# Optimization experiments

Hardware: AMD Instinct MI355X
Metric: run time of the kernel (lower is better)

The kernel has to match this reference:

```python
import jax, jax.numpy as jnp
import numpy as np

D_MODEL = 1024
N_HEADS = 16
HEAD_DIM = D_MODEL // N_HEADS
FFN = 4096
NUM_REL = 64
BATCH = 4
SEQ = 1024
EPS = 1e-6


def _layernorm(x, g, b):
    mu = jnp.mean(x, axis=-1, keepdims=True)
    var = jnp.mean(jnp.square(x - mu), axis=-1, keepdims=True)
    return (x - mu) * jax.lax.rsqrt(var + EPS) * g + b


def setup_inputs() -> dict:
    key = jax.random.key(0)
    ks = jax.random.split(key, 16)
    s_d = 1.0 / np.sqrt(D_MODEL)
    s_f = 1.0 / np.sqrt(FFN)
    inp = {
        "x": jax.random.normal(ks[0], (BATCH, SEQ, D_MODEL), jnp.float32),
        "relative_ids": jax.random.randint(ks[1], (SEQ, SEQ), 0, NUM_REL),
        # attention projections (row-major: y = x @ W + b)
        "Wq": jax.random.normal(ks[2], (D_MODEL, D_MODEL), jnp.float32) * s_d,
        "bq": jnp.zeros((D_MODEL,), jnp.float32),
        "Wk": jax.random.normal(ks[3], (D_MODEL, D_MODEL), jnp.float32) * s_d,
        "bk": jnp.zeros((D_MODEL,), jnp.float32),
        "Wv": jax.random.normal(ks[4], (D_MODEL, D_MODEL), jnp.float32) * s_d,
        "bv": jnp.zeros((D_MODEL,), jnp.float32),
        "Wo": jax.random.normal(ks[5], (D_MODEL, D_MODEL), jnp.float32) * s_d,
        "bo": jnp.zeros((D_MODEL,), jnp.float32),
        # relative position tables: Ek for keys (rel-e), Eb per-head bias (rel-b)
        "Ek": jax.random.normal(ks[6], (NUM_REL, HEAD_DIM), jnp.float32) * (1.0 / np.sqrt(HEAD_DIM)),
        "Eb": jax.random.normal(ks[7], (NUM_REL, N_HEADS), jnp.float32) * 0.02,
        # layernorms
        "g1": jnp.ones((D_MODEL,), jnp.float32),
        "b1": jnp.zeros((D_MODEL,), jnp.float32),
        "g2": jnp.ones((D_MODEL,), jnp.float32),
        "b2": jnp.zeros((D_MODEL,), jnp.float32),
        # FFN
        "W1": jax.random.normal(ks[8], (D_MODEL, FFN), jnp.float32) * s_d,
        "bf1": jnp.zeros((FFN,), jnp.float32),
        "W2": jax.random.normal(ks[9], (FFN, D_MODEL), jnp.float32) * s_f,
        "bf2": jnp.zeros((D_MODEL,), jnp.float32),
    }
    return inp


def _forward(x, relative_ids, Wq, bq, Wk, bk, Wv, bv, Wo, bo, Ek, Eb,
             g1, b1, g2, b2, W1, bf1, W2, bf2):
    B, S, D = x.shape
    # projections -> [B, H, S, Dh]
    def split_heads(t):
        return t.reshape(B, S, N_HEADS, HEAD_DIM).transpose(0, 2, 1, 3)
    q = split_heads(x @ Wq + bq)
    k = split_heads(x @ Wk + bk)
    v = split_heads(x @ Wv + bv)

    scores = jnp.einsum('bhqd,bhkd->bhqk', q, k)
    # rel-e: relative key embeddings interact with queries
    Erel = Ek[relative_ids]                      # [S, S, Dh]
    scores = scores + jnp.einsum('bhqd,qkd->bhqk', q, Erel)
    # rel-b: per-head relative bias
    scores = scores + Eb[relative_ids].transpose(2, 0, 1)[None]  # [1,H,S,S]
    scores = scores / jnp.sqrt(jnp.asarray(HEAD_DIM, x.dtype))

    attn = jax.nn.softmax(scores, axis=-1)
    ctx = jnp.einsum('bhqk,bhkd->bhqd', attn, v)
    ctx = ctx.transpose(0, 2, 1, 3).reshape(B, S, D)
    a_out = ctx @ Wo + bo

    # dropout is identity at eval
    ff_in = _layernorm(x + a_out, g1, b1)
    ff = jax.nn.relu(ff_in @ W1 + bf1) @ W2 + bf2
    return _layernorm(ff_in + ff, g2, b2)


def reference(x, relative_ids, Wq, bq, Wk, bk, Wv, bv, Wo, bo, Ek, Eb,
              g1, b1, g2, b2, W1, bf1, W2, bf2):
    return _forward(x, relative_ids, Wq, bq, Wk, bk, Wv, bv, Wo, bo, Ek, Eb,
                    g1, b1, g2, b2, W1, bf1, W2, bf2)
```

## Files before the change

### kernel.cpp

```cpp
#include <hip/hip_runtime.h>


typedef short bf16x8 __attribute__((ext_vector_type(8)));
typedef float f32x4 __attribute__((ext_vector_type(4)));

#define DEVI static __device__ __forceinline__

constexpr int SEQ = 1024, DMODEL = 1024, NH = 16, HDIM = 64, FFDIM = 4096, NREL = 64, NBATCH = 4;
constexpr int ROWS = NBATCH * SEQ;
#define QSC 0.18033688011112042f

DEVI unsigned short f2b(float f) {
  union { float f; unsigned u; } v; v.f = f;
  unsigned r = v.u + 0x7FFFu + ((v.u >> 16) & 1u);
  return (unsigned short)(r >> 16);
}

DEVI float b2f(unsigned short u) {
  union { unsigned v; float f; } x; x.v = (unsigned)u << 16; return x.f;
}

#if __has_builtin(__builtin_amdgcn_cvt_pk_bf16_f32)
DEVI unsigned pack2(float a, float b) {
  auto r = __builtin_amdgcn_cvt_pk_bf16_f32(a, b);
  return __builtin_bit_cast(unsigned, r);
}
#else
DEVI unsigned pack2(float a, float b) {
  return (unsigned)f2b(a) | ((unsigned)f2b(b) << 16);
}
#endif

DEVI float fexp2(float x) {
#if __has_builtin(__builtin_amdgcn_exp2f)
  return __builtin_amdgcn_exp2f(x);
#else
  return exp2f(x);
#endif
}

DEVI float4 ld4h(const unsigned short* p) {
  uint2 u = *(const uint2*)p;
  union { unsigned v; float f; } a, b, c, d;
  a.v = u.x << 16; b.v = u.x & 0xffff0000u; c.v = u.y << 16; d.v = u.y & 0xffff0000u;
  return make_float4(a.f, b.f, c.f, d.f);
}

DEVI void gload16(const unsigned short* g, unsigned short* l) {
  __builtin_amdgcn_global_load_lds((const __attribute__((address_space(1))) void*)g,
                                   (__attribute__((address_space(3))) void*)l, 16, 0, 0);
}

template <int BM, int BN, int WR, int WC>
DEVI void gemm_core(const unsigned short* __restrict__ A, int lda,
                    const unsigned short* __restrict__ Bt, int ldb, int K,
                    unsigned short* sA, unsigned short* sB, f32x4* acc) {
  constexpr int BK = 64;
  constexpr int MT = BM / (WR * 16), NT = BN / (WC * 16);
  const int tid = threadIdx.x;
  const int wave = tid >> 6, lane = tid & 63;
  const int wm = wave % WR, wn = wave / WR;
  const int lr = lane & 15, kq = lane >> 4;
  const int srow = lane >> 3;
  const int schunk = (lane & 7) ^ (srow & 7);
  const int sw = lr & 7;

  const f32x4 zero = {0.f, 0.f, 0.f, 0.f};
#pragma unroll
  for (int i = 0; i < MT * NT; ++i) acc[i] = zero;

  const unsigned short* ga = A + (size_t)(wave * (BM / 4) + srow) * lda + schunk * 8;
  const unsigned short* gb = Bt + (size_t)(wave * (BN / 4) + srow) * ldb + schunk * 8;
  unsigned short* la = sA + wave * (BM / 4) * BK;
  unsigned short* lb = sB + wave * (BN / 4) * BK;
  const unsigned short* pa = sA + (wm * MT * 16 + lr) * BK;
  const unsigned short* pb = sB + (wn * NT * 16 + lr) * BK;

  for (int k0 = 0; k0 < K; k0 += BK) {
#pragma unroll
    for (int j = 0; j < BM / 32; ++j) gload16(ga + (size_t)(j * 8) * lda + k0, la + j * 8 * BK);
#pragma unroll
    for (int j = 0; j < BN / 32; ++j) gload16(gb + (size_t)(j * 8) * ldb + k0, lb + j * 8 * BK);
    __syncthreads();
#pragma unroll
    for (int ks = 0; ks < 2; ++ks) {
      const int rc = ((ks * 4 + kq) ^ sw) * 8;
      bf16x8 af[MT], bv[NT];
#pragma unroll
      for (int mi = 0; mi < MT; ++mi) af[mi] = *(const bf16x8*)(pa + mi * 16 * BK + rc);
#pragma unroll
      for (int ni = 0; ni < NT; ++ni) bv[ni] = *(const bf16x8*)(pb + ni * 16 * BK + rc);
#pragma unroll
      for (int mi = 0; mi < MT; ++mi)
#pragma unroll
        for (int ni = 0; ni < NT; ++ni)
          acc[mi * NT + ni] =
              __builtin_amdgcn_mfma_f32_16x16x32_bf16(af[mi], bv[ni], acc[mi * NT + ni], 0, 0, 0);
    }
    __syncthreads();
  }
}

#define EPI_VARS                                     \
  const int tid = threadIdx.x;                       \
  const int wave = tid >> 6, lane = tid & 63;        \
  const int wm = wave % WR, wn = wave / WR;          \
  const int lr = lane & 15, kq = lane >> 4;

__global__ __launch_bounds__(256) void k_proj_qkv(
    const unsigned short* __restrict__ A, const unsigned short* __restrict__ WqT,
    const unsigned short* __restrict__ WkT, const unsigned short* __restrict__ WvT,
    const float* __restrict__ bq, const float* __restrict__ bk, const float* __restrict__ bv,
    unsigned short* __restrict__ oq, unsigned short* __restrict__ ok,
    unsigned short* __restrict__ ov) {
  constexpr int BM = 128, BN = 128, WR = 2, WC = 2, MT = 4, NT = 4;
  __shared__ __align__(16) unsigned short sA[BM * 64];
  __shared__ __align__(16) unsigned short sB[BN * 64];
  f32x4 acc[MT * NT];
  const int which = blockIdx.z;
  const unsigned short* Bt = which == 0 ? WqT : which == 1 ? WkT : WvT;
  const float* bias = which == 0 ? bq : which == 1 ? bk : bv;
  unsigned short* out = which == 0 ? oq : which == 1 ? ok : ov;
  const float scl = which == 0 ? QSC : 1.0f;
  const int m0 = blockIdx.y * BM, n0 = blockIdx.x * BN;
  gemm_core<BM, BN, WR, WC>(A + (size_t)m0 * DMODEL, DMODEL, Bt + (size_t)n0 * DMODEL, DMODEL,
                            DMODEL, sA, sB, acc);
  EPI_VARS
#pragma unroll
  for (int mi = 0; mi < MT; ++mi) {
    const int row0 = m0 + wm * MT * 16 + mi * 16 + kq * 4;
    const int b = row0 >> 10, s0 = row0 & 1023;
#pragma unroll
    for (int ni = 0; ni < NT; ++ni) {
      const int col = n0 + wn * NT * 16 + ni * 16 + lr;
      const int h = col >> 6, d = col & 63;
      const float bc = bias[col];
      f32x4 v = acc[mi * NT + ni];
#pragma unroll
      for (int r = 0; r < 4; ++r) v[r] = (v[r] + bc) * scl;
      if (which != 2) {
#pragma unroll
        for (int r = 0; r < 4; ++r)
          out[((size_t)((b * NH + h) * SEQ) + s0 + r) * HDIM + d] = f2b(v[r]);
      } else {
        uint2 p = make_uint2(pack2(v[0], v[1]), pack2(v[2], v[3]));
        *(uint2*)&out[((size_t)((b * NH + h) * HDIM) + d) * SEQ + s0] = p;
      }
    }
  }
}

template <int BM, int BN, int WR, int WC, bool RELU, bool OUTBF16, bool SPLITK = false>
__global__ __launch_bounds__(256) void k_gemm(const unsigned short* __restrict__ A, int lda,
                                              const unsigned short* __restrict__ Bt, int ldb, int K,
                                              int N, const float* __restrict__ bias,
                                              float* __restrict__ outf,
                                              unsigned short* __restrict__ outh,
                                              size_t ostride = 0) {
  constexpr int MT = BM / (WR * 16), NT = BN / (WC * 16);
  __shared__ __align__(16) unsigned short sA[BM * 64];
  __shared__ __align__(16) unsigned short sB[BN * 64];
  f32x4 acc[MT * NT];
  const int m0 = blockIdx.y * BM, n0 = blockIdx.x * BN;
  const int kc = SPLITK ? blockIdx.z : 0;
  gemm_core<BM, BN, WR, WC>(A + (size_t)m0 * lda + (size_t)kc * K, lda,
                            Bt + (size_t)n0 * ldb + (size_t)kc * K, ldb, K, sA, sB, acc);
  if (SPLITK) outh += (size_t)kc * ostride;
  EPI_VARS
#pragma unroll
  for (int mi = 0; mi < MT; ++mi) {
    const int row0 = m0 + wm * MT * 16 + mi * 16 + kq * 4;
#pragma unroll
    for (int ni = 0; ni < NT; ++ni) {
      const int col = n0 + wn * NT * 16 + ni * 16 + lr;
      const float bc = (bias && (!SPLITK || kc == 0)) ? bias[col] : 0.f;
      f32x4 v = acc[mi * NT + ni];
#pragma unroll
      for (int r = 0; r < 4; ++r) {
        float y = v[r] + bc;
        if (RELU) y = fmaxf(y, 0.f);
        if (OUTBF16 || SPLITK)
          outh[(size_t)(row0 + r) * N + col] = f2b(y);
        else
          outf[(size_t)(row0 + r) * N + col] = y;
      }
    }
  }
}

__global__ __launch_bounds__(256, 4) void k_flash(const unsigned short* __restrict__ q,
                                                  const unsigned short* __restrict__ kk,
                                                  const unsigned short* __restrict__ vT,
                                                  const unsigned short* __restrict__ Ekb,
                                                  const float* __restrict__ Eb,
                                                  const unsigned char* __restrict__ rel8,
                                                  unsigned short* __restrict__ ctx) {
  __shared__ __align__(16) unsigned short sK[128 * 64];
  __shared__ __align__(16) unsigned short sV[64 * 128];
  __shared__ __align__(16) unsigned short sqEB16[64 * 62];
  __shared__ float sRow[4][16];

  const int tid = threadIdx.x, wave = tid >> 6, lane = tid & 63;
  const int lr = lane & 15, kq = lane >> 4;

  const int L = blockIdx.y * 16 + blockIdx.x;
  const int xcd = L & 7, idx = L >> 3;
  const int z = xcd * 8 + (idx >> 4), qt = idx & 15;
  const int b = z >> 4, h = z & 15;
  const size_t zo = (size_t)z * SEQ * HDIM;
  const size_t vo = (size_t)z * HDIM * SEQ;

  const int srow8 = lane >> 3, sl8 = lane & 7;
  const int sw8 = sl8 ^ (srow8 & 7);
  const int dl = lane >> 4, sl16 = lane & 15;
  const int swl = lr & 7;
  const f32x4 zero = {0.f, 0.f, 0.f, 0.f};

  unsigned short* sQv = sV;
#pragma unroll
  for (int j = 0; j < 2; ++j) {
    const int row = wave * 16 + j * 8 + srow8;
    gload16(q + zo + (size_t)(qt * 64 + row) * 64 + sw8 * 8, sQv + (wave * 16 + j * 8) * 64);
    gload16(Ekb + (size_t)row * 64 + sw8 * 8, sK + (wave * 16 + j * 8) * 64);
  }
  __syncthreads();

  bf16x8 bq_[2];
#pragma unroll
  for (int ks = 0; ks < 2; ++ks)
    bq_[ks] = *(const bf16x8*)&sQv[(wave * 16 + lr) * 64 + (((ks * 4 + kq) ^ swl) << 3)];

  {
    f32x4 accE[4];
#pragma unroll
    for (int nf = 0; nf < 4; ++nf) accE[nf] = zero;
#pragma unroll
    for (int ks = 0; ks < 2; ++ks) {
#pragma unroll
      for (int nf = 0; nf < 4; ++nf) {
        bf16x8 ek = *(const bf16x8*)&sK[(nf * 16 + lr) * 64 + (((ks * 4 + kq) ^ swl) << 3)];
        accE[nf] = __builtin_amdgcn_mfma_f32_16x16x32_bf16(bq_[ks], ek, accE[nf], 0, 0, 0);
      }
    }
#pragma unroll
    for (int nf = 0; nf < 4; ++nf) {
      const int rid = nf * 16 + lr;
      const float eb = Eb[rid * NH + h] * QSC;
      const int base = rid * 62 + wave * 16 + kq * 4;
      *(unsigned*)&sqEB16[base] = pack2(accE[nf][0] + eb, accE[nf][1] + eb);
      *(unsigned*)&sqEB16[base + 2] = pack2(accE[nf][2] + eb, accE[nf][3] + eb);
    }
  }

  float l_run = 0.f;
  f32x4 accO[4];
#pragma unroll
  for (int nd = 0; nd < 4; ++nd) accO[nd] = zero;
  const int qrow_g = qt * 64 + wave * 16 + lr;
  const unsigned char* relrow8 = rel8 + (size_t)qrow_g * SEQ;
  const int qcol = wave * 16 + lr;
  unsigned short* sPw = sK + wave * 2048;

  for (int kt = 0; kt < 8; ++kt) {
    __syncthreads();
#pragma unroll
    for (int j = 0; j < 4; ++j) {
      const int row = wave * 32 + j * 8 + srow8;
      gload16(kk + zo + (size_t)(kt * 128 + row) * 64 + sw8 * 8, sK + (wave * 32 + j * 8) * 64);
    }
#pragma unroll
    for (int j = 0; j < 4; ++j) {
      const int row = wave * 16 + j * 4 + dl;
      const int ch = sl16 ^ (row & 15);
      gload16(vT + vo + (size_t)row * SEQ + kt * 128 + ch * 8, sV + (wave * 16 + j * 4) * 128);
    }
    unsigned ru[8];
#pragma unroll
    for (int mi = 0; mi < 8; ++mi)
      ru[mi] = *(const unsigned*)&relrow8[kt * 128 + mi * 16 + kq * 4];
    __syncthreads();

    f32x4 accS[8];
#pragma unroll
    for (int mi = 0; mi < 8; ++mi) accS[mi] = zero;
#pragma unroll
    for (int ks = 0; ks < 2; ++ks) {
#pragma unroll
      for (int mi = 0; mi < 8; ++mi) {
        bf16x8 a = *(const bf16x8*)&sK[(mi * 16 + lr) * 64 + (((ks * 4 + kq) ^ swl) << 3)];
        accS[mi] = __builtin_amdgcn_mfma_f32_16x16x32_bf16(a, bq_[ks], accS[mi], 0, 0, 0);
      }
    }
#pragma unroll
    for (int mi = 0; mi < 8; ++mi) {
      const float p0 = fexp2(accS[mi][0] + b2f(sqEB16[(int)(ru[mi] & 255u) * 62 + qcol]));
      const float p1 = fexp2(accS[mi][1] + b2f(sqEB16[(int)((ru[mi] >> 8) & 255u) * 62 + qcol]));
      const float p2 = fexp2(accS[mi][2] + b2f(sqEB16[(int)((ru[mi] >> 16) & 255u) * 62 + qcol]));
      const float p3 = fexp2(accS[mi][3] + b2f(sqEB16[(int)(ru[mi] >> 24) * 62 + qcol]));
      accS[mi][0] = p0; accS[mi][1] = p1; accS[mi][2] = p2; accS[mi][3] = p3;
      l_run += (p0 + p1) + (p2 + p3);
    }
    __syncthreads();

#pragma unroll
    for (int mi = 0; mi < 8; ++mi) {
      const int c = 2 * mi + (kq >> 1);
      *(uint2*)&sPw[lr * 128 + ((c ^ lr) << 3) + ((kq & 1) << 2)] =
          make_uint2(pack2(accS[mi][0], accS[mi][1]), pack2(accS[mi][2], accS[mi][3]));
    }
#pragma unroll
    for (int kst = 0; kst < 4; ++kst) {
      const int cc = ((kq + 4 * kst) ^ lr) << 3;
      bf16x8 a = *(const bf16x8*)&sPw[lr * 128 + cc];
#pragma unroll
      for (int nd = 0; nd < 4; ++nd) {
        bf16x8 bv = *(const bf16x8*)&sV[(nd * 16 + lr) * 128 + cc];
        accO[nd] = __builtin_amdgcn_mfma_f32_16x16x32_bf16(a, bv, accO[nd], 0, 0, 0);
      }
    }
  }

  l_run += __shfl_xor(l_run, 16);
  l_run += __shfl_xor(l_run, 32);
  if (kq == 0) sRow[wave][lr] = l_run;
  const float4 lv = *(const float4*)&sRow[wave][kq * 4];
  const float inv[4] = {1.f / lv.x, 1.f / lv.y, 1.f / lv.z, 1.f / lv.w};
  const size_t rbase = (size_t)(b * SEQ + qt * 64 + wave * 16 + kq * 4);
#pragma unroll
  for (int nd = 0; nd < 4; ++nd) {
    const int col = h * HDIM + nd * 16 + lr;
#pragma unroll
    for (int r = 0; r < 4; ++r)
      ctx[(rbase + r) * DMODEL + col] = f2b(accO[nd][r] * inv[r]);
  }
}

template <bool WB>
__global__ __launch_bounds__(256) void k_addln3(const unsigned short* __restrict__ a,
                                                const unsigned short* __restrict__ p0,
                                                const unsigned short* __restrict__ p1,
                                                const float* __restrict__ g,
                                                const float* __restrict__ beta,
                                                float* __restrict__ outf,
                                                unsigned short* __restrict__ outh) {
  const int row = blockIdx.x, t = threadIdx.x;
  const size_t base = (size_t)row * DMODEL + t * 4;
  float4 va = ld4h(&a[base]);
  float4 v0 = ld4h(&p0[base]);
  float4 v1 = ld4h(&p1[base]);
  const float x0 = va.x + v0.x + v1.x, x1 = va.y + v0.y + v1.y;
  const float x2 = va.z + v0.z + v1.z, x3 = va.w + v0.w + v1.w;
  __shared__ float red[4];
  float s = x0 + x1 + x2 + x3;
#pragma unroll
  for (int o = 32; o; o >>= 1) s += __shfl_xor(s, o);
  if ((t & 63) == 0) red[t >> 6] = s;
  __syncthreads();
  const float mu = (red[0] + red[1] + red[2] + red[3]) * (1.0f / DMODEL);
  __syncthreads();
  const float d0 = x0 - mu, d1 = x1 - mu, d2 = x2 - mu, d3 = x3 - mu;
  float qv = d0 * d0 + d1 * d1 + d2 * d2 + d3 * d3;
#pragma unroll
  for (int o = 32; o; o >>= 1) qv += __shfl_xor(qv, o);
  if ((t & 63) == 0) red[t >> 6] = qv;
  __syncthreads();
  const float var = (red[0] + red[1] + red[2] + red[3]) * (1.0f / DMODEL);
  const float sc = rsqrtf(var + 1e-6f);
  float4 vg = *(const float4*)&g[t * 4];
  float4 ve = *(const float4*)&beta[t * 4];
  float4 y;
  y.x = d0 * sc * vg.x + ve.x;
  y.y = d1 * sc * vg.y + ve.y;
  y.z = d2 * sc * vg.z + ve.z;
  y.w = d3 * sc * vg.w + ve.w;
  if (WB) {
    uint2 p = make_uint2(pack2(y.x, y.y), pack2(y.z, y.w));
    *(uint2*)&outh[base] = p;
  } else {
    *(float4*)&outf[base] = y;
  }
}

__global__ __launch_bounds__(256) void k_tcast12(
    const float* __restrict__ Wq, const float* __restrict__ Wk, const float* __restrict__ Wv,
    const float* __restrict__ Wo, const float* __restrict__ W1, const float* __restrict__ W2,
    unsigned short* __restrict__ oq, unsigned short* __restrict__ ok,
    unsigned short* __restrict__ ov, unsigned short* __restrict__ oo,
    unsigned short* __restrict__ o1, unsigned short* __restrict__ o2) {
  const int z = blockIdx.z;
  const float* in;
  unsigned short* out;
  int ldi, ldo;
  if (z < 4) {
    in = z == 0 ? Wq : z == 1 ? Wk : z == 2 ? Wv : Wo;
    out = z == 0 ? oq : z == 1 ? ok : z == 2 ? ov : oo;
    ldi = 1024; ldo = 1024;
  } else if (z < 8) {
    const int s = z - 4;
    in = W1 + (size_t)s * 1024; ldi = 4096;
    out = o1 + (size_t)s * 1024 * 1024; ldo = 1024;
  } else {
    const int s = z - 8;
    in = W2 + (size_t)s * 1024 * 1024; ldi = 1024;
    out = o2 + (size_t)s * 1024; ldo = 4096;
  }
  __shared__ float tile[32][33];
  const int tx = threadIdx.x & 31, ty = threadIdx.x >> 5;
  const int r0 = blockIdx.y * 32, c0 = blockIdx.x * 32;
#pragma unroll
  for (int i = 0; i < 4; ++i)
    tile[ty + i * 8][tx] = in[(size_t)(r0 + ty + i * 8) * ldi + c0 + tx];
  __syncthreads();
#pragma unroll
  for (int i = 0; i < 4; ++i)
    out[(size_t)(c0 + ty + i * 8) * ldo + r0 + tx] = f2b(tile[tx][ty + i * 8]);
}

__global__ __launch_bounds__(256) void k_cast2(const float* __restrict__ a,
                                               unsigned short* __restrict__ oa, int n4a,
                                               const float* __restrict__ bsrc,
                                               unsigned short* __restrict__ ob, int n4b,
                                               const int* __restrict__ rel,
                                               unsigned char* __restrict__ r8, int n4c) {
  const int i = blockIdx.x * 256 + threadIdx.x;
  if (i < n4a) {
    float4 v = *(const float4*)&a[(size_t)i * 4];
    uint2 p = make_uint2(pack2(v.x, v.y), pack2(v.z, v.w));
    *(uint2*)&oa[(size_t)i * 4] = p;
  } else {
    const int j = i - n4a;
    if (j < n4b) {
      float4 v = *(const float4*)&bsrc[(size_t)j * 4];
      uint2 p = make_uint2(pack2(v.x, v.y), pack2(v.z, v.w));
      *(uint2*)&ob[(size_t)j * 4] = p;
    } else {
      const int k2 = j - n4b;
      if (k2 < n4c) {
        int4 v = *(const int4*)&rel[(size_t)k2 * 4];
        unsigned pk = (unsigned)(v.x & 255) | ((unsigned)(v.y & 255) << 8) |
                      ((unsigned)(v.z & 255) << 16) | ((unsigned)(v.w & 255) << 24);
        *(unsigned*)&r8[(size_t)k2 * 4] = pk;
      }
    }
  }
}


extern "C" void kernel_launch(void* const* d_in, const int* in_sizes, int n_in, void* d_out,
                              int out_size, void* d_ws, size_t ws_size, hipStream_t stream) {
  const float* x = (const float*)d_in[0];
  const int* rel = (const int*)d_in[1];
  const float* Wq = (const float*)d_in[2];
  const float* bq = (const float*)d_in[3];
  const float* Wk = (const float*)d_in[4];
  const float* bk = (const float*)d_in[5];
  const float* Wv = (const float*)d_in[6];
  const float* bv = (const float*)d_in[7];
  const float* Wo = (const float*)d_in[8];
  const float* bo = (const float*)d_in[9];
  const float* Ek = (const float*)d_in[10];
  const float* Eb = (const float*)d_in[11];
  const float* g1 = (const float*)d_in[12];
  const float* b1 = (const float*)d_in[13];
  const float* g2 = (const float*)d_in[14];
  const float* b2 = (const float*)d_in[15];
  const float* W1 = (const float*)d_in[16];
  const float* bf1 = (const float*)d_in[17];
  const float* W2 = (const float*)d_in[18];
  const float* bf2 = (const float*)d_in[19];
  float* out = (float*)d_out;

  char* ws = (char*)d_ws;
  const size_t MB = 1ull << 20;
  unsigned short* Wqt = (unsigned short*)(ws + 0 * MB);
  unsigned short* Wkt = (unsigned short*)(ws + 2 * MB);
  unsigned short* Wvt = (unsigned short*)(ws + 4 * MB);
  unsigned short* Wot = (unsigned short*)(ws + 6 * MB);
  unsigned short* W1t = (unsigned short*)(ws + 8 * MB);
  unsigned short* W2t = (unsigned short*)(ws + 16 * MB);
  unsigned short* xb = (unsigned short*)(ws + 24 * MB);
  unsigned short* Ekb = (unsigned short*)(ws + 32 * MB);
  unsigned short* qbuf = (unsigned short*)(ws + 33 * MB);
  unsigned short* kbuf = (unsigned short*)(ws + 41 * MB);
  unsigned short* vTb = (unsigned short*)(ws + 49 * MB);
  unsigned short* ctx = (unsigned short*)(ws + 57 * MB);
  unsigned short* Pb = (unsigned short*)(ws + 65 * MB);
  unsigned char* rel8 = (unsigned char*)(ws + 65 * MB);
  unsigned short* ff_in_b = (unsigned short*)(ws + 81 * MB);
  unsigned short* hidden = (unsigned short*)(ws + 89 * MB);
  const size_t OST = (size_t)ROWS * DMODEL;

  k_tcast12<<<dim3(32, 32, 12), 256, 0, stream>>>(Wq, Wk, Wv, Wo, W1, W2, Wqt, Wkt, Wvt, Wot,
                                                  W1t, W2t);
  k_cast2<<<5124, 256, 0, stream>>>(x, xb, ROWS * DMODEL / 4, Ek, Ekb, NREL * HDIM / 4, rel, rel8,
                                    SEQ * SEQ / 4);

  k_proj_qkv<<<dim3(8, 32, 3), 256, 0, stream>>>(xb, Wqt, Wkt, Wvt, bq, bk, bv, qbuf, kbuf, vTb);

  k_flash<<<dim3(16, 64), 256, 0, stream>>>(qbuf, kbuf, vTb, Ekb, Eb, rel8, ctx);

  k_gemm<128, 128, 2, 2, false, true, true><<<dim3(8, 32, 2), 256, 0, stream>>>(
      ctx, DMODEL, Wot, DMODEL, DMODEL / 2, DMODEL, bo, nullptr, Pb, OST);
  k_addln3<true><<<ROWS, 256, 0, stream>>>(xb, Pb, Pb + OST, g1, b1, nullptr, ff_in_b);

  k_gemm<128, 128, 2, 2, true, true><<<dim3(32, 32), 256, 0, stream>>>(
      ff_in_b, DMODEL, W1t, DMODEL, DMODEL, FFDIM, bf1, nullptr, hidden);
  k_gemm<128, 128, 2, 2, false, true, true><<<dim3(8, 32, 2), 256, 0, stream>>>(
      hidden, FFDIM, W2t, FFDIM, FFDIM / 2, DMODEL, bf2, nullptr, Pb, OST);
  k_addln3<false><<<ROWS, 256, 0, stream>>>(ff_in_b, Pb, Pb + OST, g2, b2, out, nullptr);
}
```

Before: 374.2 us.

## Use 256x256-tile, 8-wave GEMM kernel for FFN up-projection

Result: faster. 354.2 us (-5.3%).

```diff
diff --git a/kernel.cpp b/kernel.cpp
--- a/kernel.cpp
+++ b/kernel.cpp
@@ -184,6 +184,94 @@
         else
           outf[(size_t)(row0 + r) * N + col] = y;
       }
+    }
+  }
+}
+
+__global__ __launch_bounds__(512, 2) void k_gemm256(const unsigned short* __restrict__ A, int lda,
+                                                    const unsigned short* __restrict__ Bt, int ldb,
+                                                    int K, int N, const float* __restrict__ bias,
+                                                    unsigned short* __restrict__ outh) {
+  constexpr int MT = 8, NT = 4;
+  __shared__ __align__(16) unsigned short S[2 * 32768];
+  f32x4 acc[MT * NT];
+  const int tid = threadIdx.x, wave = tid >> 6, lane = tid & 63;
+  const int wm = wave & 1, wn = wave >> 1;
+  const int lr = lane & 15, kq = lane >> 4;
+  const int srow = lane >> 3, schunk = (lane & 7) ^ (srow & 7);
+  const int sw = lr & 7;
+  const int m0 = blockIdx.y * 256, n0 = blockIdx.x * 256;
+
+  const f32x4 zero = {0.f, 0.f, 0.f, 0.f};
+#pragma unroll
+  for (int i = 0; i < MT * NT; ++i) acc[i] = zero;
+
+  const unsigned short* ga = A + (size_t)(m0 + wave * 32 + srow) * lda + schunk * 8;
+  const unsigned short* gb = Bt + (size_t)(n0 + wave * 32 + srow) * ldb + schunk * 8;
+  unsigned short* dA = S + (wave * 32) * 64;
+  unsigned short* dB = S + 16384 + (wave * 32) * 64;
+
+#define STAGE256(buf, k0)                                                              \
+  do {                                                                                 \
+    unsigned short* _a = dA + (buf) * 32768;                                           \
+    unsigned short* _b = dB + (buf) * 32768;                                           \
+    _Pragma("unroll") for (int j = 0; j < 4; ++j)                                      \
+        gload16(ga + (size_t)(j * 8) * lda + (k0), _a + j * 8 * 64);                   \
+    _Pragma("unroll") for (int j = 0; j < 4; ++j)                                      \
+        gload16(gb + (size_t)(j * 8) * ldb + (k0), _b + j * 8 * 64);                   \
+  } while (0)
+
+  STAGE256(0, 0);
+  STAGE256(1, 64);
+
+  const unsigned short* pa = S + (wm * 128 + lr) * 64;
+  const unsigned short* pb = S + 16384 + (wn * 64 + lr) * 64;
+  const int nt = K >> 6;
+
+  for (int t = 0; t < nt; ++t) {
+    const int buf = t & 1;
+    if (t < nt - 1) {
+      asm volatile("s_waitcnt vmcnt(8)" ::: "memory");
+    } else {
+      asm volatile("s_waitcnt vmcnt(0)" ::: "memory");
+    }
+    __builtin_amdgcn_s_barrier();
+    asm volatile("" ::: "memory");
+    const unsigned short* qa = pa + buf * 32768;
+    const unsigned short* qb = pb + buf * 32768;
+#pragma unroll
+    for (int ks = 0; ks < 2; ++ks) {
+      const int rc = ((ks * 4 + kq) ^ sw) * 8;
+      bf16x8 af[MT], bv[NT];
+#pragma unroll
+      for (int mi = 0; mi < MT; ++mi) af[mi] = *(const bf16x8*)(qa + mi * 16 * 64 + rc);
+#pragma unroll
+      for (int ni = 0; ni < NT; ++ni) bv[ni] = *(const bf16x8*)(qb + ni * 16 * 64 + rc);
+#pragma unroll
+      for (int mi = 0; mi < MT; ++mi)
+#pragma unroll
+        for (int ni = 0; ni < NT; ++ni)
+          acc[mi * NT + ni] =
+              __builtin_amdgcn_mfma_f32_16x16x32_bf16(af[mi], bv[ni], acc[mi * NT + ni], 0, 0, 0);
+    }
+    asm volatile("" ::: "memory");
+    __builtin_amdgcn_s_barrier();
+    asm volatile("" ::: "memory");
+    if (t + 2 < nt) STAGE256(buf, (t + 2) * 64);
+  }
+#undef STAGE256
+
+#pragma unroll
+  for (int mi = 0; mi < MT; ++mi) {
+    const int row0 = m0 + wm * 128 + mi * 16 + kq * 4;
+#pragma unroll
+    for (int ni = 0; ni < NT; ++ni) {
+      const int col = n0 + wn * 64 + ni * 16 + lr;
+      const float bc = bias[col];
+      f32x4 v = acc[mi * NT + ni];
+#pragma unroll
+      for (int r = 0; r < 4; ++r)
+        outh[(size_t)(row0 + r) * N + col] = f2b(fmaxf(v[r] + bc, 0.f));
     }
   }
 }
@@ -503,8 +591,8 @@
       ctx, DMODEL, Wot, DMODEL, DMODEL / 2, DMODEL, bo, nullptr, Pb, OST);
   k_addln3<true><<<ROWS, 256, 0, stream>>>(xb, Pb, Pb + OST, g1, b1, nullptr, ff_in_b);
 
-  k_gemm<128, 128, 2, 2, true, true><<<dim3(32, 32), 256, 0, stream>>>(
-      ff_in_b, DMODEL, W1t, DMODEL, DMODEL, FFDIM, bf1, nullptr, hidden);
+  k_gemm256<<<dim3(FFDIM / 256, ROWS / 256), 512, 0, stream>>>(ff_in_b, DMODEL, W1t, DMODEL,
+                                                               DMODEL, FFDIM, bf1, hidden);
   k_gemm<128, 128, 2, 2, false, true, true><<<dim3(8, 32, 2), 256, 0, stream>>>(
       hidden, FFDIM, W2t, FFDIM, FFDIM / 2, DMODEL, bf2, nullptr, Pb, OST);
   k_addln3<false><<<ROWS, 256, 0, stream>>>(ff_in_b, Pb, Pb + OST, g2, b2, out, nullptr);
```

## Replace GEMM core with double-buffered 256-row, 8-wave tiles using async LDS loads

Applied to the files above, without the earlier changes.

New measurement: 342.1 us. 1.09x faster.

```diff
diff --git a/kernel.cpp b/kernel.cpp
--- a/kernel.cpp
+++ b/kernel.cpp
@@ -51,45 +51,66 @@
                                    (__attribute__((address_space(3))) void*)l, 16, 0, 0);
 }
 
-template <int BM, int BN, int WR, int WC>
-DEVI void gemm_core(const unsigned short* __restrict__ A, int lda,
+template <int BM, int BN>
+DEVI void g256_core(const unsigned short* __restrict__ A, int lda,
                     const unsigned short* __restrict__ Bt, int ldb, int K,
-                    unsigned short* sA, unsigned short* sB, f32x4* acc) {
-  constexpr int BK = 64;
-  constexpr int MT = BM / (WR * 16), NT = BN / (WC * 16);
-  const int tid = threadIdx.x;
-  const int wave = tid >> 6, lane = tid & 63;
-  const int wm = wave % WR, wn = wave / WR;
+                    unsigned short* S, f32x4* acc) {
+  constexpr int MT = BM / 32, NT = BN / 64;
+  constexpr int LOADS = BM / 64 + BN / 64;
+  constexpr int SBUF = (BM + BN) * 64;
+  const int tid = threadIdx.x, wave = tid >> 6, lane = tid & 63;
+  const int wm = wave & 1, wn = wave >> 1;
   const int lr = lane & 15, kq = lane >> 4;
-  const int srow = lane >> 3;
-  const int schunk = (lane & 7) ^ (srow & 7);
+  const int srow = lane >> 3, schunk = (lane & 7) ^ (srow & 7);
   const int sw = lr & 7;
 
   const f32x4 zero = {0.f, 0.f, 0.f, 0.f};
 #pragma unroll
   for (int i = 0; i < MT * NT; ++i) acc[i] = zero;
 
-  const unsigned short* ga = A + (size_t)(wave * (BM / 4) + srow) * lda + schunk * 8;
-  const unsigned short* gb = Bt + (size_t)(wave * (BN / 4) + srow) * ldb + schunk * 8;
-  unsigned short* la = sA + wave * (BM / 4) * BK;
-  unsigned short* lb = sB + wave * (BN / 4) * BK;
-  const unsigned short* pa = sA + (wm * MT * 16 + lr) * BK;
-  const unsigned short* pb = sB + (wn * NT * 16 + lr) * BK;
-
-  for (int k0 = 0; k0 < K; k0 += BK) {
-#pragma unroll
-    for (int j = 0; j < BM / 32; ++j) gload16(ga + (size_t)(j * 8) * lda + k0, la + j * 8 * BK);
-#pragma unroll
-    for (int j = 0; j < BN / 32; ++j) gload16(gb + (size_t)(j * 8) * ldb + k0, lb + j * 8 * BK);
-    __syncthreads();
+  const unsigned short* ga = A + (size_t)(wave * (BM / 8) + srow) * lda + schunk * 8;
+  const unsigned short* gb = Bt + (size_t)(wave * (BN / 8) + srow) * ldb + schunk * 8;
+  unsigned short* dA = S + wave * (BM / 8) * 64;
+  unsigned short* dB = S + BM * 64 + wave * (BN / 8) * 64;
+
+#define STG(buf, k0)                                                         \
+  do {                                                                       \
+    _Pragma("unroll") for (int j = 0; j < BM / 64; ++j)                      \
+        gload16(ga + (size_t)(j * 8) * lda + (k0), dA + (buf)*SBUF + j * 8 * 64); \
+    _Pragma("unroll") for (int j = 0; j < BN / 64; ++j)                      \
+        gload16(gb + (size_t)(j * 8) * ldb + (k0), dB + (buf)*SBUF + j * 8 * 64); \
+  } while (0)
+
+  STG(0, 0);
+  STG(1, 64);
+
+  const unsigned short* pa = S + (wm * (BM / 2) + lr) * 64;
+  const unsigned short* pb = S + BM * 64 + (wn * (BN / 4) + lr) * 64;
+  const int nt = K >> 6;
+
+  for (int t = 0; t < nt; ++t) {
+    const int buf = t & 1;
+    if (t < nt - 1) {
+      if constexpr (LOADS == 8) {
+        asm volatile("s_waitcnt vmcnt(8)" ::: "memory");
+      } else {
+        asm volatile("s_waitcnt vmcnt(6)" ::: "memory");
+      }
+    } else {
+      asm volatile("s_waitcnt vmcnt(0)" ::: "memory");
+    }
+    __builtin_amdgcn_s_barrier();
+    asm volatile("" ::: "memory");
+    const unsigned short* qa = pa + buf * SBUF;
+    const unsigned short* qb = pb + buf * SBUF;
 #pragma unroll
     for (int ks = 0; ks < 2; ++ks) {
       const int rc = ((ks * 4 + kq) ^ sw) * 8;
       bf16x8 af[MT], bv[NT];
 #pragma unroll
-      for (int mi = 0; mi < MT; ++mi) af[mi] = *(const bf16x8*)(pa + mi * 16 * BK + rc);
-#pragma unroll
-      for (int ni = 0; ni < NT; ++ni) bv[ni] = *(const bf16x8*)(pb + ni * 16 * BK + rc);
+      for (int mi = 0; mi < MT; ++mi) af[mi] = *(const bf16x8*)(qa + mi * 16 * 64 + rc);
+#pragma unroll
+      for (int ni = 0; ni < NT; ++ni) bv[ni] = *(const bf16x8*)(qb + ni * 16 * 64 + rc);
 #pragma unroll
       for (int mi = 0; mi < MT; ++mi)
 #pragma unroll
@@ -97,45 +118,76 @@
           acc[mi * NT + ni] =
               __builtin_amdgcn_mfma_f32_16x16x32_bf16(af[mi], bv[ni], acc[mi * NT + ni], 0, 0, 0);
     }
-    __syncthreads();
-  }
-}
-
-#define EPI_VARS                                     \
-  const int tid = threadIdx.x;                       \
-  const int wave = tid >> 6, lane = tid & 63;        \
-  const int wm = wave % WR, wn = wave / WR;          \
-  const int lr = lane & 15, kq = lane >> 4;
-
-__global__ __launch_bounds__(256) void k_proj_qkv(
+    asm volatile("" ::: "memory");
+    __builtin_amdgcn_s_barrier();
+    asm volatile("" ::: "memory");
+    if (t + 2 < nt) STG(buf, (t + 2) * 64);
+  }
+#undef STG
+}
+
+template <int BN2, bool RELU, bool SPLITK>
+__global__ __launch_bounds__(512, 2) void k_g256(const unsigned short* __restrict__ A, int lda,
+                                                 const unsigned short* __restrict__ Bt, int ldb,
+                                                 int K, int N, const float* __restrict__ bias,
+                                                 unsigned short* __restrict__ outh,
+                                                 size_t ostride) {
+  constexpr int BM = 256, MT = 8, NT = BN2 / 64;
+  __shared__ __align__(16) unsigned short S[2 * (BM + BN2) * 64];
+  f32x4 acc[MT * NT];
+  const int m0 = blockIdx.y * BM, n0 = blockIdx.x * BN2;
+  const int kc = SPLITK ? blockIdx.z : 0;
+  g256_core<BM, BN2>(A + (size_t)m0 * lda + (size_t)kc * K, lda,
+                     Bt + (size_t)n0 * ldb + (size_t)kc * K, ldb, K, S, acc);
+  if (SPLITK) outh += (size_t)kc * ostride;
+  const int tid = threadIdx.x, wave = tid >> 6, lane = tid & 63;
+  const int wm = wave & 1, wn = wave >> 1, lr = lane & 15, kq = lane >> 4;
+#pragma unroll
+  for (int mi = 0; mi < MT; ++mi) {
+    const int row0 = m0 + wm * 128 + mi * 16 + kq * 4;
+#pragma unroll
+    for (int ni = 0; ni < NT; ++ni) {
+      const int col = n0 + wn * (BN2 / 4) + ni * 16 + lr;
+      const float bc = (!SPLITK || kc == 0) ? bias[col] : 0.f;
+      f32x4 v = acc[mi * NT + ni];
+#pragma unroll
+      for (int r = 0; r < 4; ++r) {
+        float y = v[r] + bc;
+        if (RELU) y = fmaxf(y, 0.f);
+        outh[(size_t)(row0 + r) * N + col] = f2b(y);
+      }
+    }
+  }
+}
+
+__global__ __launch_bounds__(512, 2) void k_proj256(
     const unsigned short* __restrict__ A, const unsigned short* __restrict__ WqT,
     const unsigned short* __restrict__ WkT, const unsigned short* __restrict__ WvT,
     const float* __restrict__ bq, const float* __restrict__ bk, const float* __restrict__ bv,
     unsigned short* __restrict__ oq, unsigned short* __restrict__ ok,
     unsigned short* __restrict__ ov) {
-  constexpr int BM = 128, BN = 128, WR = 2, WC = 2, MT = 4, NT = 4;
-  __shared__ __align__(16) unsigned short sA[BM * 64];
-  __shared__ __align__(16) unsigned short sB[BN * 64];
-  f32x4 acc[MT * NT];
+  __shared__ __align__(16) unsigned short S[2 * 512 * 64];
+  f32x4 acc[32];
   const int which = blockIdx.z;
   const unsigned short* Bt = which == 0 ? WqT : which == 1 ? WkT : WvT;
   const float* bias = which == 0 ? bq : which == 1 ? bk : bv;
   unsigned short* out = which == 0 ? oq : which == 1 ? ok : ov;
   const float scl = which == 0 ? QSC : 1.0f;
-  const int m0 = blockIdx.y * BM, n0 = blockIdx.x * BN;
-  gemm_core<BM, BN, WR, WC>(A + (size_t)m0 * DMODEL, DMODEL, Bt + (size_t)n0 * DMODEL, DMODEL,
-                            DMODEL, sA, sB, acc);
-  EPI_VARS
-#pragma unroll
-  for (int mi = 0; mi < MT; ++mi) {
-    const int row0 = m0 + wm * MT * 16 + mi * 16 + kq * 4;
+  const int m0 = blockIdx.y * 256, n0 = blockIdx.x * 256;
+  g256_core<256, 256>(A + (size_t)m0 * DMODEL, DMODEL, Bt + (size_t)n0 * DMODEL, DMODEL, DMODEL,
+                      S, acc);
+  const int tid = threadIdx.x, wave = tid >> 6, lane = tid & 63;
+  const int wm = wave & 1, wn = wave >> 1, lr = lane & 15, kq = lane >> 4;
+#pragma unroll
+  for (int mi = 0; mi < 8; ++mi) {
+    const int row0 = m0 + wm * 128 + mi * 16 + kq * 4;
     const int b = row0 >> 10, s0 = row0 & 1023;
 #pragma unroll
-    for (int ni = 0; ni < NT; ++ni) {
-      const int col = n0 + wn * NT * 16 + ni * 16 + lr;
+    for (int ni = 0; ni < 4; ++ni) {
+      const int col = n0 + wn * 64 + ni * 16 + lr;
       const int h = col >> 6, d = col & 63;
       const float bc = bias[col];
-      f32x4 v = acc[mi * NT + ni];
+      f32x4 v = acc[mi * 4 + ni];
 #pragma unroll
       for (int r = 0; r < 4; ++r) v[r] = (v[r] + bc) * scl;
       if (which != 2) {
@@ -145,44 +197,6 @@
       } else {
         uint2 p = make_uint2(pack2(v[0], v[1]), pack2(v[2], v[3]));
         *(uint2*)&out[((size_t)((b * NH + h) * HDIM) + d) * SEQ + s0] = p;
-      }
-    }
-  }
-}
-
-template <int BM, int BN, int WR, int WC, bool RELU, bool OUTBF16, bool SPLITK = false>
-__global__ __launch_bounds__(256) void k_gemm(const unsigned short* __restrict__ A, int lda,
-                                              const unsigned short* __restrict__ Bt, int ldb, int K,
-                                              int N, const float* __restrict__ bias,
-                                              float* __restrict__ outf,
-                                              unsigned short* __restrict__ outh,
-                                              size_t ostride = 0) {
-  constexpr int MT = BM / (WR * 16), NT = BN / (WC * 16);
-  __shared__ __align__(16) unsigned short sA[BM * 64];
-  __shared__ __align__(16) unsigned short sB[BN * 64];
-  f32x4 acc[MT * NT];
-  const int m0 = blockIdx.y * BM, n0 = blockIdx.x * BN;
-  const int kc = SPLITK ? blockIdx.z : 0;
-  gemm_core<BM, BN, WR, WC>(A + (size_t)m0 * lda + (size_t)kc * K, lda,
-                            Bt + (size_t)n0 * ldb + (size_t)kc * K, ldb, K, sA, sB, acc);
-  if (SPLITK) outh += (size_t)kc * ostride;
-  EPI_VARS
-#pragma unroll
-  for (int mi = 0; mi < MT; ++mi) {
-    const int row0 = m0 + wm * MT * 16 + mi * 16 + kq * 4;
-#pragma unroll
-    for (int ni = 0; ni < NT; ++ni) {
-      const int col = n0 + wn * NT * 16 + ni * 16 + lr;
-      const float bc = (bias && (!SPLITK || kc == 0)) ? bias[col] : 0.f;
-      f32x4 v = acc[mi * NT + ni];
-#pragma unroll
-      for (int r = 0; r < 4; ++r) {
-        float y = v[r] + bc;
-        if (RELU) y = fmaxf(y, 0.f);
-        if (OUTBF16 || SPLITK)
-          outh[(size_t)(row0 + r) * N + col] = f2b(y);
-        else
-          outf[(size_t)(row0 + r) * N + col] = y;
       }
     }
   }
@@ -495,17 +509,17 @@
   k_cast2<<<5124, 256, 0, stream>>>(x, xb, ROWS * DMODEL / 4, Ek, Ekb, NREL * HDIM / 4, rel, rel8,
                                     SEQ * SEQ / 4);
 
-  k_proj_qkv<<<dim3(8, 32, 3), 256, 0, stream>>>(xb, Wqt, Wkt, Wvt, bq, bk, bv, qbuf, kbuf, vTb);
+  k_proj256<<<dim3(4, 16, 3), 512, 0, stream>>>(xb, Wqt, Wkt, Wvt, bq, bk, bv, qbuf, kbuf, vTb);
 
   k_flash<<<dim3(16, 64), 256, 0, stream>>>(qbuf, kbuf, vTb, Ekb, Eb, rel8, ctx);
 
-  k_gemm<128, 128, 2, 2, false, true, true><<<dim3(8, 32, 2), 256, 0, stream>>>(
-      ctx, DMODEL, Wot, DMODEL, DMODEL / 2, DMODEL, bo, nullptr, Pb, OST);
+  k_g256<128, false, true><<<dim3(8, 16, 2), 512, 0, stream>>>(ctx, DMODEL, Wot, DMODEL,
+                                                               DMODEL / 2, DMODEL, bo, Pb, OST);
   k_addln3<true><<<ROWS, 256, 0, stream>>>(xb, Pb, Pb + OST, g1, b1, nullptr, ff_in_b);
 
-  k_gemm<128, 128, 2, 2, true, true><<<dim3(32, 32), 256, 0, stream>>>(
-      ff_in_b, DMODEL, W1t, DMODEL, DMODEL, FFDIM, bf1, nullptr, hidden);
-  k_gemm<128, 128, 2, 2, false, true, true><<<dim3(8, 32, 2), 256, 0, stream>>>(
-      hidden, FFDIM, W2t, FFDIM, FFDIM / 2, DMODEL, bf2, nullptr, Pb, OST);
+  k_g256<256, true, false><<<dim3(FFDIM / 256, ROWS / 256), 512, 0, stream>>>(
+      ff_in_b, DMODEL, W1t, DMODEL, DMODEL, FFDIM, bf1, hidden, 0);
+  k_g256<128, false, true><<<dim3(8, 16, 2), 512, 0, stream>>>(hidden, FFDIM, W2t, FFDIM,
+                                                               FFDIM / 2, DMODEL, bf2, Pb, OST);
   k_addln3<false><<<ROWS, 256, 0, stream>>>(ff_in_b, Pb, Pb + OST, g2, b2, out, nullptr);
 }
```
